# Kernel tuning notes

Hardware: AMD Instinct MI355X
Metric: run time of the kernel (lower is better)

## Reference

```python
import jax, jax.numpy as jnp
import numpy as np

NB_COMP = 8
LAT_DIM = 512
NB_NEUR = 1024
OUT_DIM = 512
N_SAMPLES = 16384


def setup_inputs() -> dict:
    key = jax.random.key(0)
    ks = jax.random.split(key, 8)
    s1 = 1.0 / np.sqrt(LAT_DIM)
    s2 = 1.0 / np.sqrt(NB_NEUR)
    return {
        "epsilon": jax.random.normal(ks[0], (N_SAMPLES, LAT_DIM), dtype=jnp.float32),
        "comp_idx": jax.random.randint(ks[1], (N_SAMPLES,), 0, NB_COMP, dtype=jnp.int32),
        "mu": jnp.zeros((NB_COMP, LAT_DIM), dtype=jnp.float32),
        "rho": jnp.zeros((NB_COMP,), dtype=jnp.float32),  # sigma = softplus(rho)
        "W1": jax.random.normal(ks[2], (NB_COMP, LAT_DIM, NB_NEUR), dtype=jnp.float32) * s1,
        "b1": jax.random.normal(ks[3], (NB_COMP, NB_NEUR), dtype=jnp.float32) * s1,
        "W2": jax.random.normal(ks[4], (NB_COMP, NB_NEUR, OUT_DIM), dtype=jnp.float32) * s2,
        "b2": jax.random.normal(ks[5], (NB_COMP, OUT_DIM), dtype=jnp.float32) * s2,
    }


def reference(epsilon, comp_idx, mu, rho, W1, b1, W2, b2):
    # GNNens.forward: per-sample categorical component dispatch through a
    # 1-hidden-layer sigmoid MLP. Vectorized as compute-all-components + select.
    sigma = jax.nn.softplus(rho)                          # [C]
    # lat_c[c,n,d] = epsilon[n,d] * sigma[c] + mu[c,d]
    lat = epsilon[None, :, :] * sigma[:, None, None] + mu[:, None, :]  # [C,N,D]
    h = jax.nn.sigmoid(jnp.einsum('cnd,cdh->cnh', lat, W1) + b1[:, None, :])  # [C,N,H]
    y = jnp.einsum('cnh,cho->cno', h, W2) + b2[:, None, :]                    # [C,N,O]
    # select each sample's routed component
    idx = comp_idx[None, :, None].astype(jnp.int32)       # [1,N,1]
    out = jnp.take_along_axis(y, idx, axis=0)[0]          # [N,O]
    return out
```

## Files before the change

### kernel.cpp

```cpp
#include <hip/hip_runtime.h>
#include <stdint.h>

#define NCOMP 8
#define LATD  512
#define HID   1024
#define OUTD  512
#define NS    16384

typedef unsigned short u16;
typedef __bf16 bf16x8 __attribute__((ext_vector_type(8)));
typedef float  f32x4  __attribute__((ext_vector_type(4)));

#define MAPS       (NS/128 + NCOMP)
#define SLOT_CHUNK ((MAPS + 7)/8)

#define ORDER_OFF  2048
#define APACK_OFF  (ORDER_OFF + NS*4)
#define W1T_OFF    (APACK_OFF + (size_t)NS*LATD*2)
#define W2T_OFF    (W1T_OFF + (size_t)NCOMP*LATD*HID*2)
#define H_OFF      (W2T_OFF + (size_t)NCOMP*HID*OUTD*2)
#define WS_NEEDED  (H_OFF + (size_t)NS*HID*2)

__device__ __forceinline__ u16 f2b(float f) {
  unsigned int u = __builtin_bit_cast(unsigned int, f);
  u = (u + 0x7FFFu + ((u >> 16) & 1u)) >> 16;
  return (u16)u;
}

__device__ __forceinline__ void load_lds16(const void* g, void* l) {
  __builtin_amdgcn_global_load_lds((const __attribute__((address_space(1))) void*)g,
                                   (__attribute__((address_space(3))) void*)l, 16, 0, 0);
}

__global__ __launch_bounds__(1024)
void k_prep_all(const int* __restrict__ idx, const float* __restrict__ rho,
                const float* __restrict__ eps, const float* __restrict__ mu,
                const float* __restrict__ W1, const float* __restrict__ W2,
                int* __restrict__ offsets, int* __restrict__ ntiles,
                int* __restrict__ map, int* __restrict__ order,
                u16* __restrict__ Apack, u16* __restrict__ W1T, u16* __restrict__ W2T) {
  __shared__ float tile[64][65];
  __shared__ int hist_s[NCOMP];
  __shared__ int wtot[16];
  const int b = blockIdx.x;
  const int t = threadIdx.x;

  if (b < NCOMP) {
    const int c = b;
    const int wave = t >> 6, lane = t & 63;

    int my[16];
    #pragma unroll
    for (int i = 0; i < 16; ++i) my[i] = idx[t + (i << 10)];

    unsigned long long nib = 0;
    #pragma unroll
    for (int i = 0; i < 16; ++i) nib += 1ull << (my[i] << 2);

    if (t < NCOMP) hist_s[t] = 0;
    __syncthreads();

    #pragma unroll
    for (int cc = 0; cc < NCOMP; ++cc) {
      int v = (int)((nib >> (cc << 2)) & 15);
      #pragma unroll
      for (int d = 1; d < 64; d <<= 1) v += __shfl_xor(v, d);
      if (lane == 0) atomicAdd(&hist_s[cc], v);
    }

    int v = (int)((nib >> (c << 2)) & 15);
    int s = v;
    #pragma unroll
    for (int d = 1; d < 64; d <<= 1) {
      int u = __shfl_up(s, d);
      if (lane >= d) s += u;
    }
    if (lane == 63) wtot[wave] = s;
    __syncthreads();

    int wbase = 0;
    for (int w = 0; w < wave; ++w) wbase += wtot[w];
    int off_c = 0;
    #pragma unroll
    for (int cc = 0; cc < NCOMP; ++cc) if (cc < c) off_c += hist_s[cc];

    int pos = off_c + wbase + (s - v);
    #pragma unroll
    for (int i = 0; i < 16; ++i)
      if (my[i] == c) order[pos++] = t + (i << 10);

    if (t == 0) {
      if (c == 0) {
        int a = 0;
        for (int cc = 0; cc < NCOMP; ++cc) { offsets[cc] = a; a += hist_s[cc]; }
        offsets[NCOMP] = a;
        int tot = 0;
        for (int cc = 0; cc < NCOMP; ++cc) tot += (hist_s[cc] + 127) >> 7;
        ntiles[0] = tot;
      }
      int mb = 0;
      for (int cc = 0; cc < c; ++cc) mb += (hist_s[cc] + 127) >> 7;
      int nt = (hist_s[c] + 127) >> 7;
      for (int m = 0; m < nt; ++m) map[mb + m] = (c << 16) | m;
    }
  } else if (b < NCOMP + 1024) {
    int g = (b - NCOMP) * 1024 + t;
    int i = g >> 6;
    int d = (g & 63) << 3;
    int c = idx[i];
    float r = rho[c];
    float sg = (r > 20.f) ? r : log1pf(expf(r));
    const float4* ep = reinterpret_cast<const float4*>(eps + (size_t)i*LATD + d);
    const float4* mp = reinterpret_cast<const float4*>(mu  + (size_t)c*LATD + d);
    float4 e0 = ep[0], e1 = ep[1], m0 = mp[0], m1 = mp[1];
    unsigned o0 = f2b(e0.x*sg+m0.x), o1 = f2b(e0.y*sg+m0.y), o2 = f2b(e0.z*sg+m0.z), o3 = f2b(e0.w*sg+m0.w);
    unsigned o4 = f2b(e1.x*sg+m1.x), o5 = f2b(e1.y*sg+m1.y), o6 = f2b(e1.z*sg+m1.z), o7 = f2b(e1.w*sg+m1.w);
    uint4 pk;
    pk.x = o0 | (o1<<16); pk.y = o2 | (o3<<16); pk.z = o4 | (o5<<16); pk.w = o6 | (o7<<16);
    *reinterpret_cast<uint4*>(Apack + (size_t)i*LATD + d) = pk;
  } else {
    int bb = b - (NCOMP + 1024);
    const float* src; u16* dst; int CC, r0, c0;
    int R;
    if (bb < 1024) {
      int comp = bb >> 7, loc = bb & 127;
      R = LATD; CC = HID;
      c0 = (loc & 15) << 6; r0 = (loc >> 4) << 6;
      src = W1 + (size_t)comp*R*CC; dst = W1T + (size_t)comp*R*CC;
    } else {
      int b2 = bb - 1024;
      int comp = b2 >> 7, loc = b2 & 127;
      R = HID; CC = OUTD;
      c0 = (loc & 7) << 6; r0 = (loc >> 3) << 6;
      src = W2 + (size_t)comp*R*CC; dst = W2T + (size_t)comp*R*CC;
    }
    int tx = t & 63, ty = t >> 6;
    for (int rr = ty; rr < 64; rr += 16)
      tile[rr][tx] = src[(size_t)(r0+rr)*CC + c0 + tx];
    __syncthreads();
    int cc = t >> 4, ch = t & 15;
    float f0 = tile[(ch<<2)+0][cc];
    float f1 = tile[(ch<<2)+1][cc];
    float g2 = tile[(ch<<2)+2][cc];
    float g3 = tile[(ch<<2)+3][cc];
    uint2 pk;
    pk.x = (unsigned)f2b(f0) | ((unsigned)f2b(f1) << 16);
    pk.y = (unsigned)f2b(g2) | ((unsigned)f2b(g3) << 16);
    *reinterpret_cast<uint2*>(&dst[(size_t)(c0+cc)*R + r0 + (ch<<2)]) = pk;
  }
}

template<int K, int NB, int STAGE>
__global__ __launch_bounds__(256, 4)
void k_gemm(const u16* __restrict__ A, const u16* __restrict__ BT,
            const int* __restrict__ offsets, const int* __restrict__ ntiles,
            const int* __restrict__ map, const int* __restrict__ order,
            const float* __restrict__ bias,
            u16* __restrict__ Hout, float* __restrict__ Yout) {
  constexpr int NCB = NB/128;
  __shared__ u16 As[128*64];
  __shared__ u16 Bs[128*64];
  __shared__ int ord[128];

  const int id    = blockIdx.x;
  const int xcd   = id & 7;
  const int sub   = id >> 3;
  const int ncolb = sub % NCB;
  const int slot  = xcd*SLOT_CHUNK + sub / NCB;
  if (slot >= ntiles[0]) return;
  const int packed = map[slot];
  const int c      = packed >> 16;
  const int bstart = offsets[c];
  const int bend   = offsets[c+1];
  const int tile0  = bstart + (packed & 0xffff)*128;
  const int ncol0  = ncolb*128;

  const int tid  = threadIdx.x;
  const int wave = tid >> 6;
  const int lane = tid & 63;
  const int srow = (wave<<5) + (lane>>3);
  const int scol = ((lane & 7) ^ ((lane >> 3) & 7)) << 3;

  if (STAGE == 2 && tid < 128) {
    int gr = tile0 + tid;
    ord[tid] = order[gr < bend ? gr : bstart];
  }

  size_t a_off[4], b_off[4];
  const size_t bbase = (size_t)c * NB * K;
  #pragma unroll
  for (int i = 0; i < 4; ++i) {
    int ar = tile0 + srow + (i<<3);
    if (ar >= bend) ar = bend - 1;
    int arow = (STAGE == 1) ? order[ar] : ar;
    a_off[i] = (size_t)arow * K + scol;
    b_off[i] = bbase + (size_t)(ncol0 + srow + (i<<3)) * K + scol;
  }

  const int wr   = (wave >> 1) << 6;
  const int wc   = (wave & 1) << 6;
  const int quad = lane >> 4;
  const int l16  = lane & 15;
  const int sw   = l16 & 7;

  f32x4 acc[4][4] = {};

  for (int k0 = 0; k0 < K; k0 += 64) {
    #pragma unroll
    for (int i = 0; i < 4; ++i)
      load_lds16(A + a_off[i] + k0, &As[((wave<<5) + (i<<3))<<6]);
    #pragma unroll
    for (int i = 0; i < 4; ++i)
      load_lds16(BT + b_off[i] + k0, &Bs[((wave<<5) + (i<<3))<<6]);
    __syncthreads();
    #pragma unroll
    for (int kk = 0; kk < 64; kk += 32) {
      const int kc = (kk >> 3) + quad;
      const int sc = (kc ^ sw) << 3;
      bf16x8 af[4], bfr[4];
      #pragma unroll
      for (int mi = 0; mi < 4; ++mi)
        af[mi] = *reinterpret_cast<const bf16x8*>(&As[((wr + (mi<<4) + l16)<<6) + sc]);
      #pragma unroll
      for (int ni = 0; ni < 4; ++ni)
        bfr[ni] = *reinterpret_cast<const bf16x8*>(&Bs[((wc + (ni<<4) + l16)<<6) + sc]);
      #pragma unroll
      for (int ni = 0; ni < 4; ++ni)
        #pragma unroll
        for (int mi = 0; mi < 4; ++mi)
          acc[ni][mi] = __builtin_amdgcn_mfma_f32_16x16x32_bf16(bfr[ni], af[mi], acc[ni][mi], 0, 0, 0);
    }
    __syncthreads();
  }

  f32x4 bias4[4];
  #pragma unroll
  for (int ni = 0; ni < 4; ++ni)
    bias4[ni] = *reinterpret_cast<const f32x4*>(
        &bias[(size_t)c*NB + ncol0 + wc + (ni<<4) + (quad<<2)]);

  #pragma unroll
  for (int mi = 0; mi < 4; ++mi) {
    const int row_l = wr + (mi<<4) + l16;
    const int grow  = tile0 + row_l;
    if (grow < bend) {
      #pragma unroll
      for (int ni = 0; ni < 4; ++ni) {
        const int col = ncol0 + wc + (ni<<4) + (quad<<2);
        float v0 = acc[ni][mi][0] + bias4[ni][0];
        float v1 = acc[ni][mi][1] + bias4[ni][1];
        float v2 = acc[ni][mi][2] + bias4[ni][2];
        float v3 = acc[ni][mi][3] + bias4[ni][3];
        if (STAGE == 1) {
          v0 = __builtin_amdgcn_rcpf(1.0f + __expf(-v0));
          v1 = __builtin_amdgcn_rcpf(1.0f + __expf(-v1));
          v2 = __builtin_amdgcn_rcpf(1.0f + __expf(-v2));
          v3 = __builtin_amdgcn_rcpf(1.0f + __expf(-v3));
          uint2 pk;
          pk.x = (unsigned)f2b(v0) | ((unsigned)f2b(v1) << 16);
          pk.y = (unsigned)f2b(v2) | ((unsigned)f2b(v3) << 16);
          *reinterpret_cast<uint2*>(&Hout[(size_t)grow*NB + col]) = pk;
        } else {
          float4 o; o.x = v0; o.y = v1; o.z = v2; o.w = v3;
          *reinterpret_cast<float4*>(&Yout[(size_t)ord[row_l]*NB + col]) = o;
        }
      }
    }
  }
}

__global__ void k_naive(const float* __restrict__ eps, const int* __restrict__ idx,
                        const float* __restrict__ mu, const float* __restrict__ rho,
                        const float* __restrict__ W1, const float* __restrict__ b1,
                        const float* __restrict__ W2, const float* __restrict__ b2,
                        float* __restrict__ out) {
  __shared__ float lat[LATD];
  __shared__ float h[HID];
  int n = blockIdx.x, t = threadIdx.x;
  int c = idx[n];
  float r = rho[c];
  float sg = (r > 20.f) ? r : log1pf(expf(r));
  for (int d = t; d < LATD; d += 256) lat[d] = eps[(size_t)n*LATD+d]*sg + mu[(size_t)c*LATD+d];
  __syncthreads();
  for (int j = t; j < HID; j += 256) {
    float a = b1[(size_t)c*HID+j];
    const float* w = W1 + (size_t)c*LATD*HID + j;
    for (int d = 0; d < LATD; ++d) a += lat[d]*w[(size_t)d*HID];
    h[j] = 1.f/(1.f+expf(-a));
  }
  __syncthreads();
  for (int o = t; o < OUTD; o += 256) {
    float a = b2[(size_t)c*OUTD+o];
    const float* w = W2 + (size_t)c*HID*OUTD + o;
    for (int j = 0; j < HID; ++j) a += h[j]*w[(size_t)j*OUTD];
    out[(size_t)n*OUTD+o] = a;
  }
}

extern "C" void kernel_launch(void* const* d_in, const int* in_sizes, int n_in,
                              void* d_out, int out_size, void* d_ws, size_t ws_size,
                              hipStream_t stream) {
  const float* eps = (const float*)d_in[0];
  const int*   idx = (const int*)d_in[1];
  const float* mu  = (const float*)d_in[2];
  const float* rho = (const float*)d_in[3];
  const float* W1  = (const float*)d_in[4];
  const float* b1  = (const float*)d_in[5];
  const float* W2  = (const float*)d_in[6];
  const float* b2  = (const float*)d_in[7];
  float* out = (float*)d_out;

  if (ws_size < WS_NEEDED) {
    k_naive<<<NS, 256, 0, stream>>>(eps, idx, mu, rho, W1, b1, W2, b2, out);
    return;
  }

  char* ws = (char*)d_ws;
  int*   offsets = (int*)(ws + 0);
  int*   ntiles  = (int*)(ws + 96);
  int*   map     = (int*)(ws + 128);
  int*   order   = (int*)(ws + ORDER_OFF);
  u16*   Apack   = (u16*)(ws + APACK_OFF);
  u16*   W1T     = (u16*)(ws + W1T_OFF);
  u16*   W2T     = (u16*)(ws + W2T_OFF);
  u16*   Hws     = (u16*)(ws + H_OFF);

  k_prep_all<<<NCOMP + 1024 + 2048, 1024, 0, stream>>>(
      idx, rho, eps, mu, W1, W2, offsets, ntiles, map, order, Apack, W1T, W2T);
  k_gemm<LATD, HID, 1><<<8*SLOT_CHUNK*(HID/128), 256, 0, stream>>>(
      Apack, W1T, offsets, ntiles, map, order, b1, Hws, nullptr);
  k_gemm<HID, OUTD, 2><<<8*SLOT_CHUNK*(OUTD/128), 256, 0, stream>>>(
      Hws, W2T, offsets, ntiles, map, order, b2, nullptr, out);
}
```

Measured before the change: 184.3 us.

## Overlap W2 transpose with first GEMM and shrink prep blocks to 256 threads

Moves the W2 fp32-to-bf16 transpose out of the prep kernel and into extra blocks of the first GEMM launch, sharing LDS through a union. The transpose then runs alongside GEMM1 instead of ahead of it. The prep kernel now uses 256-thread blocks: the histogram packs 16-bit counters into two 64-bit words, and each pack block handles 8 rows. The aim is to shorten the prep critical path and fill idle CUs during GEMM1. The cost is extra blocks competing with GEMM1, and the histogram re-reads idx from global memory.

Result: slower. 196.2 us (+6.4%).

```diff
diff --git a/kernel.cpp b/kernel.cpp
--- a/kernel.cpp
+++ b/kernel.cpp
@@ -21,6 +21,12 @@
 #define H_OFF      (W2T_OFF + (size_t)NCOMP*HID*OUTD*2)
 #define WS_NEEDED  (H_OFF + (size_t)NS*HID*2)
 
+#define PACK_B0   8
+#define PACK_NB   2048
+#define W1T_B0    (PACK_B0 + PACK_NB)
+#define PREP_NB   (W1T_B0 + 1024)
+#define G1_JOBS   (8*SLOT_CHUNK*(HID/128))
+
 __device__ __forceinline__ u16 f2b(float f) {
   unsigned int u = __builtin_bit_cast(unsigned int, f);
   u = (u + 0x7FFFu + ((u >> 16) & 1u)) >> 16;
@@ -32,49 +38,68 @@
                                    (__attribute__((address_space(3))) void*)l, 16, 0, 0);
 }
 
-__global__ __launch_bounds__(1024)
-void k_prep_all(const int* __restrict__ idx, const float* __restrict__ rho,
-                const float* __restrict__ eps, const float* __restrict__ mu,
-                const float* __restrict__ W1, const float* __restrict__ W2,
-                int* __restrict__ offsets, int* __restrict__ ntiles,
-                int* __restrict__ map, int* __restrict__ order,
-                u16* __restrict__ Apack, u16* __restrict__ W1T, u16* __restrict__ W2T) {
-  __shared__ float tile[64][65];
+__device__ __forceinline__
+void wtrans64(const float* __restrict__ src, u16* __restrict__ dst,
+              int CC, int R, int c0, int r0, float* tile ) {
+  const int t = threadIdx.x;
+  const int tx = t & 63, ty = t >> 6;
+  for (int rr = ty; rr < 64; rr += 4)
+    tile[rr*65 + tx] = src[(size_t)(r0+rr)*CC + c0 + tx];
+  __syncthreads();
+  const int ch = t & 15;
+  #pragma unroll
+  for (int q = 0; q < 4; ++q) {
+    const int cc = (t >> 4) + (q << 4);
+    float f0 = tile[((ch<<2)+0)*65 + cc];
+    float f1 = tile[((ch<<2)+1)*65 + cc];
+    float f2 = tile[((ch<<2)+2)*65 + cc];
+    float f3 = tile[((ch<<2)+3)*65 + cc];
+    uint2 pk;
+    pk.x = (unsigned)f2b(f0) | ((unsigned)f2b(f1) << 16);
+    pk.y = (unsigned)f2b(f2) | ((unsigned)f2b(f3) << 16);
+    *reinterpret_cast<uint2*>(&dst[(size_t)(c0+cc)*R + r0 + (ch<<2)]) = pk;
+  }
+}
+
+__global__ __launch_bounds__(256)
+void k_prep(const int* __restrict__ idx, const float* __restrict__ rho,
+            const float* __restrict__ eps, const float* __restrict__ mu,
+            const float* __restrict__ W1,
+            int* __restrict__ offsets, int* __restrict__ ntiles,
+            int* __restrict__ map, int* __restrict__ order,
+            u16* __restrict__ Apack, u16* __restrict__ W1T) {
+  __shared__ float tile[64*65];
   __shared__ int hist_s[NCOMP];
-  __shared__ int wtot[16];
+  __shared__ int wtot[4];
   const int b = blockIdx.x;
   const int t = threadIdx.x;
 
   if (b < NCOMP) {
     const int c = b;
     const int wave = t >> 6, lane = t & 63;
-
-    int my[16];
-    #pragma unroll
-    for (int i = 0; i < 16; ++i) my[i] = idx[t + (i << 10)];
-
-    unsigned long long nib = 0;
-    #pragma unroll
-    for (int i = 0; i < 16; ++i) nib += 1ull << (my[i] << 2);
-
+    unsigned long long lo = 0, hi = 0;
+    for (int i = 0; i < 64; ++i) {
+      int v = idx[t + (i << 8)];
+      unsigned long long one = 1ull << ((v & 3) << 4);
+      if (v < 4) lo += one; else hi += one;
+    }
     if (t < NCOMP) hist_s[t] = 0;
     __syncthreads();
 
-    #pragma unroll
-    for (int cc = 0; cc < NCOMP; ++cc) {
-      int v = (int)((nib >> (cc << 2)) & 15);
-      #pragma unroll
-      for (int d = 1; d < 64; d <<= 1) v += __shfl_xor(v, d);
-      if (lane == 0) atomicAdd(&hist_s[cc], v);
-    }
-
-    int v = (int)((nib >> (c << 2)) & 15);
+    unsigned long long rlo = lo, rhi = hi;
+    #pragma unroll
+    for (int d = 1; d < 64; d <<= 1) { rlo += __shfl_xor(rlo, d); rhi += __shfl_xor(rhi, d); }
+    if (lane == 0) {
+      #pragma unroll
+      for (int cc = 0; cc < 4; ++cc) atomicAdd(&hist_s[cc],   (int)((rlo >> (cc<<4)) & 0xffff));
+      #pragma unroll
+      for (int cc = 0; cc < 4; ++cc) atomicAdd(&hist_s[cc+4], (int)((rhi >> (cc<<4)) & 0xffff));
+    }
+
+    int v = (int)(((c < 4 ? lo : hi) >> ((c & 3) << 4)) & 0xffff);
     int s = v;
     #pragma unroll
-    for (int d = 1; d < 64; d <<= 1) {
-      int u = __shfl_up(s, d);
-      if (lane >= d) s += u;
-    }
+    for (int d = 1; d < 64; d <<= 1) { int u = __shfl_up(s, d); if (lane >= d) s += u; }
     if (lane == 63) wtot[wave] = s;
     __syncthreads();
 
@@ -85,9 +110,10 @@
     for (int cc = 0; cc < NCOMP; ++cc) if (cc < c) off_c += hist_s[cc];
 
     int pos = off_c + wbase + (s - v);
-    #pragma unroll
-    for (int i = 0; i < 16; ++i)
-      if (my[i] == c) order[pos++] = t + (i << 10);
+    for (int i = 0; i < 64; ++i) {
+      int smp = t + (i << 8);
+      if (idx[smp] == c) order[pos++] = smp;
+    }
 
     if (t == 0) {
       if (c == 0) {
@@ -103,66 +129,41 @@
       int nt = (hist_s[c] + 127) >> 7;
       for (int m = 0; m < nt; ++m) map[mb + m] = (c << 16) | m;
     }
-  } else if (b < NCOMP + 1024) {
-    int g = (b - NCOMP) * 1024 + t;
-    int i = g >> 6;
-    int d = (g & 63) << 3;
-    int c = idx[i];
-    float r = rho[c];
-    float sg = (r > 20.f) ? r : log1pf(expf(r));
-    const float4* ep = reinterpret_cast<const float4*>(eps + (size_t)i*LATD + d);
-    const float4* mp = reinterpret_cast<const float4*>(mu  + (size_t)c*LATD + d);
-    float4 e0 = ep[0], e1 = ep[1], m0 = mp[0], m1 = mp[1];
-    unsigned o0 = f2b(e0.x*sg+m0.x), o1 = f2b(e0.y*sg+m0.y), o2 = f2b(e0.z*sg+m0.z), o3 = f2b(e0.w*sg+m0.w);
-    unsigned o4 = f2b(e1.x*sg+m1.x), o5 = f2b(e1.y*sg+m1.y), o6 = f2b(e1.z*sg+m1.z), o7 = f2b(e1.w*sg+m1.w);
-    uint4 pk;
-    pk.x = o0 | (o1<<16); pk.y = o2 | (o3<<16); pk.z = o4 | (o5<<16); pk.w = o6 | (o7<<16);
-    *reinterpret_cast<uint4*>(Apack + (size_t)i*LATD + d) = pk;
+  } else if (b < W1T_B0) {
+    const int base = (b - PACK_B0) << 3;
+    #pragma unroll
+    for (int it = 0; it < 2; ++it) {
+      int i = base + (it << 2) + (t >> 6);
+      int d = (t & 63) << 3;
+      int c = idx[i];
+      float r = rho[c];
+      float sg = (r > 20.f) ? r : log1pf(expf(r));
+      const float4* ep = reinterpret_cast<const float4*>(eps + (size_t)i*LATD + d);
+      const float4* mp = reinterpret_cast<const float4*>(mu  + (size_t)c*LATD + d);
+      float4 e0 = ep[0], e1 = ep[1], m0 = mp[0], m1 = mp[1];
+      unsigned o0 = f2b(e0.x*sg+m0.x), o1 = f2b(e0.y*sg+m0.y), o2 = f2b(e0.z*sg+m0.z), o3 = f2b(e0.w*sg+m0.w);
+      unsigned o4 = f2b(e1.x*sg+m1.x), o5 = f2b(e1.y*sg+m1.y), o6 = f2b(e1.z*sg+m1.z), o7 = f2b(e1.w*sg+m1.w);
+      uint4 pk;
+      pk.x = o0 | (o1<<16); pk.y = o2 | (o3<<16); pk.z = o4 | (o5<<16); pk.w = o6 | (o7<<16);
+      *reinterpret_cast<uint4*>(Apack + (size_t)i*LATD + d) = pk;
+    }
   } else {
-    int bb = b - (NCOMP + 1024);
-    const float* src; u16* dst; int CC, r0, c0;
-    int R;
-    if (bb < 1024) {
-      int comp = bb >> 7, loc = bb & 127;
-      R = LATD; CC = HID;
-      c0 = (loc & 15) << 6; r0 = (loc >> 4) << 6;
-      src = W1 + (size_t)comp*R*CC; dst = W1T + (size_t)comp*R*CC;
-    } else {
-      int b2 = bb - 1024;
-      int comp = b2 >> 7, loc = b2 & 127;
-      R = HID; CC = OUTD;
-      c0 = (loc & 7) << 6; r0 = (loc >> 3) << 6;
-      src = W2 + (size_t)comp*R*CC; dst = W2T + (size_t)comp*R*CC;
-    }
-    int tx = t & 63, ty = t >> 6;
-    for (int rr = ty; rr < 64; rr += 16)
-      tile[rr][tx] = src[(size_t)(r0+rr)*CC + c0 + tx];
-    __syncthreads();
-    int cc = t >> 4, ch = t & 15;
-    float f0 = tile[(ch<<2)+0][cc];
-    float f1 = tile[(ch<<2)+1][cc];
-    float g2 = tile[(ch<<2)+2][cc];
-    float g3 = tile[(ch<<2)+3][cc];
-    uint2 pk;
-    pk.x = (unsigned)f2b(f0) | ((unsigned)f2b(f1) << 16);
-    pk.y = (unsigned)f2b(g2) | ((unsigned)f2b(g3) << 16);
-    *reinterpret_cast<uint2*>(&dst[(size_t)(c0+cc)*R + r0 + (ch<<2)]) = pk;
+    int bb = b - W1T_B0;
+    int comp = bb >> 7, loc = bb & 127;
+    wtrans64(W1 + (size_t)comp*LATD*HID, W1T + (size_t)comp*LATD*HID,
+             HID, LATD, (loc & 15) << 6, (loc >> 4) << 6, tile);
   }
 }
 
 template<int K, int NB, int STAGE>
-__global__ __launch_bounds__(256, 4)
-void k_gemm(const u16* __restrict__ A, const u16* __restrict__ BT,
-            const int* __restrict__ offsets, const int* __restrict__ ntiles,
-            const int* __restrict__ map, const int* __restrict__ order,
-            const float* __restrict__ bias,
-            u16* __restrict__ Hout, float* __restrict__ Yout) {
+__device__ __forceinline__
+void gemm_tile(const int id, const u16* __restrict__ A, const u16* __restrict__ BT,
+               const int* __restrict__ offsets, const int* __restrict__ ntiles,
+               const int* __restrict__ map, const int* __restrict__ order,
+               const float* __restrict__ bias,
+               u16* __restrict__ Hout, float* __restrict__ Yout,
+               u16* As, u16* Bs, int* ord) {
   constexpr int NCB = NB/128;
-  __shared__ u16 As[128*64];
-  __shared__ u16 Bs[128*64];
-  __shared__ int ord[128];
-
-  const int id    = blockIdx.x;
   const int xcd   = id & 7;
   const int sub   = id >> 3;
   const int ncolb = sub % NCB;
@@ -269,6 +270,44 @@
   }
 }
 
+union __attribute__((aligned(16))) SmemU {
+  struct { u16 As[128*64]; u16 Bs[128*64]; } g;
+  float tile[64*65];
+};
+
+__global__ __launch_bounds__(256, 4)
+void k_g1w2t(const u16* __restrict__ Apack, const u16* __restrict__ W1T,
+             const float* __restrict__ W2,
+             const int* __restrict__ offsets, const int* __restrict__ ntiles,
+             const int* __restrict__ map, const int* __restrict__ order,
+             const float* __restrict__ b1,
+             u16* __restrict__ Hout, u16* __restrict__ W2T) {
+  __shared__ SmemU sm;
+  __shared__ int ord[128];
+  const int id = blockIdx.x;
+  if (id < G1_JOBS) {
+    gemm_tile<LATD, HID, 1>(id, Apack, W1T, offsets, ntiles, map, order, b1,
+                            Hout, nullptr, sm.g.As, sm.g.Bs, ord);
+  } else {
+    int bb = id - G1_JOBS;
+    int comp = bb >> 7, loc = bb & 127;
+    wtrans64(W2 + (size_t)comp*HID*OUTD, W2T + (size_t)comp*HID*OUTD,
+             OUTD, HID, (loc & 7) << 6, (loc >> 3) << 6, sm.tile);
+  }
+}
+
+__global__ __launch_bounds__(256, 4)
+void k_gemm2(const u16* __restrict__ Hws, const u16* __restrict__ W2T,
+             const int* __restrict__ offsets, const int* __restrict__ ntiles,
+             const int* __restrict__ map, const int* __restrict__ order,
+             const float* __restrict__ b2, float* __restrict__ Yout) {
+  __shared__ __attribute__((aligned(16))) u16 As[128*64];
+  __shared__ __attribute__((aligned(16))) u16 Bs[128*64];
+  __shared__ int ord[128];
+  gemm_tile<HID, OUTD, 2>(blockIdx.x, Hws, W2T, offsets, ntiles, map, order, b2,
+                          nullptr, Yout, As, Bs, ord);
+}
+
 __global__ void k_naive(const float* __restrict__ eps, const int* __restrict__ idx,
                         const float* __restrict__ mu, const float* __restrict__ rho,
                         const float* __restrict__ W1, const float* __restrict__ b1,
@@ -325,10 +364,10 @@
   u16*   W2T     = (u16*)(ws + W2T_OFF);
   u16*   Hws     = (u16*)(ws + H_OFF);
 
-  k_prep_all<<<NCOMP + 1024 + 2048, 1024, 0, stream>>>(
-      idx, rho, eps, mu, W1, W2, offsets, ntiles, map, order, Apack, W1T, W2T);
-  k_gemm<LATD, HID, 1><<<8*SLOT_CHUNK*(HID/128), 256, 0, stream>>>(
-      Apack, W1T, offsets, ntiles, map, order, b1, Hws, nullptr);
-  k_gemm<HID, OUTD, 2><<<8*SLOT_CHUNK*(OUTD/128), 256, 0, stream>>>(
-      Hws, W2T, offsets, ntiles, map, order, b2, nullptr, out);
-}
+  k_prep<<<PREP_NB, 256, 0, stream>>>(
+      idx, rho, eps, mu, W1, offsets, ntiles, map, order, Apack, W1T);
+  k_g1w2t<<<G1_JOBS + 1024, 256, 0, stream>>>(
+      Apack, W1T, W2, offsets, ntiles, map, order, b1, Hws, W2T);
+  k_gemm2<<<8*SLOT_CHUNK*(OUTD/128), 256, 0, stream>>>(
+      Hws, W2T, offsets, ntiles, map, order, b2, out);
+}
```
